# Kernel tuning notes

Hardware: AMD Instinct MI355X
Metric: run time of the kernel (lower is better)

Reference implementation:

```python
import jax, jax.numpy as jnp
import numpy as np

N = 100000      # nodes
E = 1600000     # edges (avg degree 16)
F_IN = 128      # node feature dim
F_E = 8         # edge feature dim
H = 4           # attention heads (layer 1)
C = 16          # hidden per head
T = 1           # target size (layer 2, heads=1, concat=False)
NEG_SLOPE = 0.2


def setup_inputs() -> dict:
    key = jax.random.key(0)
    ks = jax.random.split(key, 20)
    g = lambda k, shape, fan: (jax.random.normal(k, shape, jnp.float32) / np.sqrt(fan))
    return {
        "x": jax.random.normal(ks[0], (N, F_IN), jnp.float32),
        "edge_index": jax.random.randint(ks[1], (2, E), 0, N, dtype=jnp.int32),
        "edge_attr": jax.random.normal(ks[2], (E, F_E), jnp.float32),
        # layer 1 (in=F_IN, out=C, heads=H, concat=True, edge_dim=F_E)
        "Wl1": g(ks[3], (F_IN, H * C), F_IN),
        "bl1": jnp.zeros((H * C,), jnp.float32),
        "Wr1": g(ks[4], (F_IN, H * C), F_IN),
        "br1": jnp.zeros((H * C,), jnp.float32),
        "We1": g(ks[5], (F_E, H * C), F_E),
        "att1": g(ks[6], (H, C), C),
        "b1": jnp.zeros((H * C,), jnp.float32),
        # layer 2 (in=H*C, out=T, heads=1, concat=False, edge_dim=F_E)
        "Wl2": g(ks[7], (H * C, T), H * C),
        "bl2": jnp.zeros((T,), jnp.float32),
        "Wr2": g(ks[8], (H * C, T), H * C),
        "br2": jnp.zeros((T,), jnp.float32),
        "We2": g(ks[9], (F_E, T), F_E),
        "att2": g(ks[10], (1, T), T),
        "b2": jnp.zeros((T,), jnp.float32),
    }


def _gatv2(x, src, dst, eattr, Wl, bl, Wr, br, We, att, bias, heads, out_ch, concat, n_nodes):
    # add self loops, self-loop edge_attr = mean of edge_attr (PyG fill_value='mean')
    loop = jnp.arange(n_nodes, dtype=src.dtype)
    src_a = jnp.concatenate([src, loop])
    dst_a = jnp.concatenate([dst, loop])
    ea = jnp.concatenate(
        [eattr, jnp.broadcast_to(eattr.mean(axis=0), (n_nodes, eattr.shape[1]))], axis=0)

    xl = (x @ Wl + bl).reshape(n_nodes, heads, out_ch)   # source transform
    xr = (x @ Wr + br).reshape(n_nodes, heads, out_ch)   # target transform
    ee = (ea @ We).reshape(-1, heads, out_ch)            # edge transform (no bias)

    # GATv2: score = att . LeakyReLU(x_l[src] + x_r[dst] + W_e e)
    s = jax.nn.leaky_relu(xl[src_a] + xr[dst_a] + ee, NEG_SLOPE)  # [Ea,H,C]
    logits = jnp.einsum('ehc,hc->eh', s, att)                      # [Ea,H]

    # segment softmax over destination nodes (every node has a self loop)
    m = jax.ops.segment_max(logits, dst_a, num_segments=n_nodes)   # [N,H]
    p = jnp.exp(logits - m[dst_a])
    denom = jax.ops.segment_sum(p, dst_a, num_segments=n_nodes)
    alpha = p / denom[dst_a]                                        # [Ea,H]

    out = jax.ops.segment_sum(xl[src_a] * alpha[:, :, None], dst_a,
                              num_segments=n_nodes)                 # [N,H,C]
    out = out.reshape(n_nodes, heads * out_ch) if concat else out.mean(axis=1)
    return out + bias


def reference(x, edge_index, edge_attr, Wl1, bl1, Wr1, br1, We1, att1, b1,
              Wl2, bl2, Wr2, br2, We2, att2, b2):
    src, dst = edge_index[0], edge_index[1]
    # dropout layers are identity at eval time (training=False)
    h = _gatv2(x, src, dst, edge_attr, Wl1, bl1, Wr1, br1, We1, att1, b1,
               H, C, True, N)
    h = jax.nn.elu(h)
    out = _gatv2(h, src, dst, edge_attr, Wl2, bl2, Wr2, br2, We2, att2, b2,
                 1, T, False, N)
    return out
```

## Files before the change

### kernel.cpp

```cpp
#include <hip/hip_runtime.h>
#include <hip/hip_fp16.h>
#include <math.h>

#define N_NODES 100000
#define N_EDGES 1600000
#define N_ITEMS (N_EDGES + N_NODES)
#define F_IN 128
#define HC 64
#define NEG 0.2f
#define SCAN_BS 1024
#define SCAN_NB ((N_NODES + SCAN_BS - 1) / SCAN_BS)
#define MS_BLOCKS 1024

union H2I { __half2 h; int i; };
typedef int v2i __attribute__((ext_vector_type(2)));
typedef int v4i __attribute__((ext_vector_type(4)));

__device__ __forceinline__ float4 h4_to_f4(v2i w) {
    H2I u0, u1; u0.i = w.x; u1.i = w.y;
    float2 a = __half22float2(u0.h), b = __half22float2(u1.h);
    return make_float4(a.x, a.y, b.x, b.y);
}
__device__ __forceinline__ float4 h8_lo(v4i r) {
    H2I h0, h1; h0.i = r.x; h1.i = r.y;
    float2 f0 = __half22float2(h0.h), f1 = __half22float2(h1.h);
    return make_float4(f0.x, f0.y, f1.x, f1.y);
}
__device__ __forceinline__ float4 h8_hi(v4i r) {
    H2I h2, h3; h2.i = r.z; h3.i = r.w;
    float2 f2 = __half22float2(h2.h), f3 = __half22float2(h3.h);
    return make_float4(f2.x, f2.y, f3.x, f3.y);
}

__global__ void mean_sum_kernel(const float* __restrict__ ea, const int* __restrict__ dst,
                                float* __restrict__ partials, unsigned* __restrict__ deg) {
    __shared__ float sh[4][8];
    int stride = gridDim.x * blockDim.x;
    float acc[8] = {0.f,0.f,0.f,0.f,0.f,0.f,0.f,0.f};
    for (int r = blockIdx.x * blockDim.x + threadIdx.x; r < N_EDGES; r += stride) {
        const float4* p = (const float4*)(ea + (size_t)r * 8);
        float4 a = p[0], b = p[1];
        acc[0] += a.x; acc[1] += a.y; acc[2] += a.z; acc[3] += a.w;
        acc[4] += b.x; acc[5] += b.y; acc[6] += b.z; acc[7] += b.w;
        atomicAdd(&deg[dst[r]], 1u);
    }
    int wid  = threadIdx.x >> 6;
    int lane = threadIdx.x & 63;
#pragma unroll
    for (int k = 0; k < 8; k++) {
        float v = acc[k];
        for (int off = 32; off; off >>= 1) v += __shfl_down(v, off);
        if (lane == 0) sh[wid][k] = v;
    }
    __syncthreads();
    if (threadIdx.x < 8) {
        float s = sh[0][threadIdx.x] + sh[1][threadIdx.x] + sh[2][threadIdx.x] + sh[3][threadIdx.x];
        partials[blockIdx.x * 8 + threadIdx.x] = s;
    }
}

__global__ void scan1(const unsigned* __restrict__ deg, unsigned* __restrict__ local_inc,
                      unsigned* __restrict__ bsum,
                      const float* __restrict__ partials, float* __restrict__ sum8) {
    if (blockIdx.x == 0 && threadIdx.x < 64) {
        int lane = threadIdx.x;
        int c = lane & 7, g = lane >> 3;
        float s = 0.f;
        for (int b = g; b < MS_BLOCKS; b += 8) s += partials[b * 8 + c];
        s += __shfl_xor(s, 8);
        s += __shfl_xor(s, 16);
        s += __shfl_xor(s, 32);
        if (lane < 8) sum8[lane] = s;
    }
    __shared__ unsigned wsum[16];
    int i = blockIdx.x * SCAN_BS + threadIdx.x;
    int lane = threadIdx.x & 63;
    int wid  = threadIdx.x >> 6;
    unsigned v = (i < N_NODES) ? (deg[i] + 1u) : 0u;
    unsigned sc = v;
#pragma unroll
    for (int off = 1; off < 64; off <<= 1) {
        unsigned t = __shfl_up(sc, off);
        if (lane >= off) sc += t;
    }
    if (lane == 63) wsum[wid] = sc;
    __syncthreads();
    if (threadIdx.x < 16) {
        unsigned w = wsum[threadIdx.x];
#pragma unroll
        for (int off = 1; off < 16; off <<= 1) {
            unsigned t = __shfl_up(w, off);
            if ((int)threadIdx.x >= off) w += t;
        }
        wsum[threadIdx.x] = w;
    }
    __syncthreads();
    unsigned base = wid ? wsum[wid - 1] : 0u;
    sc += base;
    if (i < N_NODES) local_inc[i] = sc;
    if (threadIdx.x == SCAN_BS - 1) bsum[blockIdx.x] = sc;
}

__global__ void scan23(const unsigned* __restrict__ local_inc, const unsigned* __restrict__ deg,
                       const unsigned* __restrict__ bsum,
                       unsigned* __restrict__ row_start, unsigned* __restrict__ next) {
    __shared__ unsigned tmp[128];
    int t = threadIdx.x;
    if (t < 128) tmp[t] = (t < SCAN_NB) ? bsum[t] : 0u;
    __syncthreads();
    for (int off = 1; off < 128; off <<= 1) {
        unsigned add = 0u;
        if (t < 128 && t >= off) add = tmp[t - off];
        __syncthreads();
        if (t < 128) tmp[t] += add;
        __syncthreads();
    }
    int i = blockIdx.x * blockDim.x + t;
    if (i >= N_NODES) return;
    int b = i >> 10;
    unsigned base = b ? tmp[b - 1] : 0u;
    unsigned v = local_inc[i] - (deg[i] + 1u) + base;
    row_start[i] = v;
    next[i] = v;
}

__global__ void scatter_kernel(const int* __restrict__ src, const int* __restrict__ dst,
                               const float* __restrict__ ea, const float* __restrict__ sum8,
                               const float* __restrict__ We2,
                               unsigned* __restrict__ next,
                               int* __restrict__ rec, __half* __restrict__ seah) {
    int item = blockIdx.x * blockDim.x + threadIdx.x;
    if (item >= N_ITEMS) return;
    int s, d;
    float4 a, b;
    if (item < N_EDGES) {
        s = src[item]; d = dst[item];
        const float4* p = (const float4*)(ea + (size_t)item * 8);
        a = p[0]; b = p[1];
    } else {
        s = d = item - N_EDGES;
        const float inv = 1.0f / N_EDGES;
        a = make_float4(sum8[0]*inv, sum8[1]*inv, sum8[2]*inv, sum8[3]*inv);
        b = make_float4(sum8[4]*inv, sum8[5]*inv, sum8[6]*inv, sum8[7]*inv);
    }
    float ee2 = a.x*We2[0] + a.y*We2[1] + a.z*We2[2] + a.w*We2[3]
              + b.x*We2[4] + b.y*We2[5] + b.z*We2[6] + b.w*We2[7];
    unsigned pos = atomicAdd(&next[d], 1u);
    v2i rr; rr.x = s; rr.y = __float_as_int(ee2);
    *(v2i*)(rec + (size_t)pos * 2) = rr;
    H2I p0, p1, p2, p3;
    p0.h = __floats2half2_rn(a.x, a.y);
    p1.h = __floats2half2_rn(a.z, a.w);
    p2.h = __floats2half2_rn(b.x, b.y);
    p3.h = __floats2half2_rn(b.z, b.w);
    *(int4*)(seah + (size_t)pos * 8) = make_int4(p0.i, p1.i, p2.i, p3.i);
}

__global__ __launch_bounds__(256) void gemm1_kernel(
        const float* __restrict__ x,
        const float* __restrict__ Wl, const float* __restrict__ bl,
        const float* __restrict__ Wr, const float* __restrict__ br,
        __half* __restrict__ xlh, float* __restrict__ xr) {
    __shared__ float xs_t[F_IN][36];
    int t = threadIdx.x & 31;
    int g = threadIdx.x >> 5;
    const float* Wsel = (t < 16) ? Wl : Wr;
    const float* bsel = (t < 16) ? bl : br;
    int jc = (t < 16) ? 4 * t : 4 * t - HC;
    float4 bias = *(const float4*)(bsel + jc);

    int n0 = blockIdx.x * 32;
    int row = threadIdx.x >> 3;
    int cq  = threadIdx.x & 7;
#pragma unroll
    for (int r = 0; r < 4; r++) {
        int c = cq * 4 + r * 32;
        float4 v = *(const float4*)(x + (size_t)(n0 + row) * F_IN + c);
        xs_t[c + 0][row] = v.x;
        xs_t[c + 1][row] = v.y;
        xs_t[c + 2][row] = v.z;
        xs_t[c + 3][row] = v.w;
    }
    __syncthreads();
    int nb = g * 4;
    float4 a0 = bias, a1 = bias, a2 = bias, a3 = bias;
#pragma unroll 4
    for (int k = 0; k < F_IN; k++) {
        float4 w  = *(const float4*)(Wsel + k * HC + jc);
        float4 xv = *(const float4*)&xs_t[k][nb];
        a0.x += w.x * xv.x; a0.y += w.y * xv.x; a0.z += w.z * xv.x; a0.w += w.w * xv.x;
        a1.x += w.x * xv.y; a1.y += w.y * xv.y; a1.z += w.z * xv.y; a1.w += w.w * xv.y;
        a2.x += w.x * xv.z; a2.y += w.y * xv.z; a2.z += w.z * xv.z; a2.w += w.w * xv.z;
        a3.x += w.x * xv.w; a3.y += w.y * xv.w; a3.z += w.z * xv.w; a3.w += w.w * xv.w;
    }
    if (t < 16) {
        float4 arr[4] = {a0, a1, a2, a3};
#pragma unroll
        for (int r = 0; r < 4; r++) {
            H2I u0, u1;
            u0.h = __floats2half2_rn(arr[r].x, arr[r].y);
            u1.h = __floats2half2_rn(arr[r].z, arr[r].w);
            *(int2*)(xlh + (size_t)(n0 + nb + r) * HC + jc) = make_int2(u0.i, u1.i);
        }
    } else {
        *(float4*)(xr + (size_t)(n0 + nb + 0) * HC + jc) = a0;
        *(float4*)(xr + (size_t)(n0 + nb + 1) * HC + jc) = a1;
        *(float4*)(xr + (size_t)(n0 + nb + 2) * HC + jc) = a2;
        *(float4*)(xr + (size_t)(n0 + nb + 3) * HC + jc) = a3;
    }
}

__device__ __forceinline__ void edge_update_nm(const float4* __restrict__ we,
                                               const float4& attv, const float4& xrv,
                                               bool valid, const float4& ea0, const float4& ea1,
                                               const float4& xlv,
                                               float& den, float4& acc) {
    float4 v;
    v.x = xlv.x + xrv.x + ea0.x*we[0].x + ea0.y*we[1].x + ea0.z*we[2].x + ea0.w*we[3].x
                        + ea1.x*we[4].x + ea1.y*we[5].x + ea1.z*we[6].x + ea1.w*we[7].x;
    v.y = xlv.y + xrv.y + ea0.x*we[0].y + ea0.y*we[1].y + ea0.z*we[2].y + ea0.w*we[3].y
                        + ea1.x*we[4].y + ea1.y*we[5].y + ea1.z*we[6].y + ea1.w*we[7].y;
    v.z = xlv.z + xrv.z + ea0.x*we[0].z + ea0.y*we[1].z + ea0.z*we[2].z + ea0.w*we[3].z
                        + ea1.x*we[4].z + ea1.y*we[5].z + ea1.z*we[6].z + ea1.w*we[7].z;
    v.w = xlv.w + xrv.w + ea0.x*we[0].w + ea0.y*we[1].w + ea0.z*we[2].w + ea0.w*we[3].w
                        + ea1.x*we[4].w + ea1.y*we[5].w + ea1.z*we[6].w + ea1.w*we[7].w;
    v.x = fmaxf(v.x, NEG * v.x);
    v.y = fmaxf(v.y, NEG * v.y);
    v.z = fmaxf(v.z, NEG * v.z);
    v.w = fmaxf(v.w, NEG * v.w);
    float prod = v.x*attv.x + v.y*attv.y + v.z*attv.z + v.w*attv.w;
    prod += __shfl_xor(prod, 1);
    prod += __shfl_xor(prod, 2);
    float p = valid ? __expf(prod) : 0.f;
    den   += p;
    acc.x += p * xlv.x;
    acc.y += p * xlv.y;
    acc.z += p * xlv.z;
    acc.w += p * xlv.w;
}

__global__ void gat1_kernel(const unsigned* __restrict__ row_start, const unsigned* __restrict__ deg,
                            const int* __restrict__ rec, const __half* __restrict__ seah,
                            const float* __restrict__ We1, const float* __restrict__ att1,
                            const float* __restrict__ b1,
                            const __half* __restrict__ xlh, const float* __restrict__ xr,
                            const float* __restrict__ Wl2, const float* __restrict__ bl2,
                            const float* __restrict__ Wr2, const float* __restrict__ br2,
                            float* __restrict__ xl2, float* __restrict__ xr2) {
    int node = blockIdx.x * (blockDim.x >> 6) + (threadIdx.x >> 6);
    int lane = threadIdx.x & 63;
    if (node >= N_NODES) return;
    int g  = lane >> 4;
    int cl = lane & 15;
    unsigned start = row_start[node];
    unsigned cnt   = deg[node] + 1u;
    unsigned cm1   = cnt - 1u;

    float4 we[8];
#pragma unroll
    for (int k = 0; k < 8; k++) we[k] = *(const float4*)(We1 + k * HC + 4 * cl);
    float4 attv = *(const float4*)(att1 + 4 * cl);
    float4 xrv  = *(const float4*)(xr + (size_t)node * HC + 4 * cl);

    float denA = 0.f, denB = 0.f;
    float4 accA = make_float4(0.f,0.f,0.f,0.f), accB = make_float4(0.f,0.f,0.f,0.f);

#define IDXA(J) (start + min((J) + (unsigned)g, cm1))
#define IDXB(J) (start + min((J) + 4u + (unsigned)g, cm1))
    unsigned iA = IDXA(0u), iB = IDXB(0u);
    v2i rA = __builtin_nontemporal_load((const v2i*)(rec + (size_t)iA * 2));
    v2i rB = __builtin_nontemporal_load((const v2i*)(rec + (size_t)iB * 2));
    v4i spA = __builtin_nontemporal_load((const v4i*)(seah + (size_t)iA * 8));
    v4i spB = __builtin_nontemporal_load((const v4i*)(seah + (size_t)iB * 8));
    v2i xpA = *(const v2i*)(xlh + (size_t)rA.x * HC + 4 * cl);
    v2i xpB = *(const v2i*)(xlh + (size_t)rB.x * HC + 4 * cl);

    for (unsigned j = 0; j < cnt; j += 8) {
        float4 e0A = h8_lo(spA), e1A = h8_hi(spA), xA = h4_to_f4(xpA);
        float4 e0B = h8_lo(spB), e1B = h8_hi(spB), xB = h4_to_f4(xpB);
        bool vA = (j + g) < cnt, vB = (j + 4 + g) < cnt;
        if (j + 8 < cnt) {
            iA = IDXA(j + 8); iB = IDXB(j + 8);
            rA = __builtin_nontemporal_load((const v2i*)(rec + (size_t)iA * 2));
            rB = __builtin_nontemporal_load((const v2i*)(rec + (size_t)iB * 2));
            spA = __builtin_nontemporal_load((const v4i*)(seah + (size_t)iA * 8));
            spB = __builtin_nontemporal_load((const v4i*)(seah + (size_t)iB * 8));
            xpA = *(const v2i*)(xlh + (size_t)rA.x * HC + 4 * cl);
            xpB = *(const v2i*)(xlh + (size_t)rB.x * HC + 4 * cl);
        }
        edge_update_nm(we, attv, xrv, vA, e0A, e1A, xA, denA, accA);
        edge_update_nm(we, attv, xrv, vB, e0B, e1B, xB, denB, accB);
    }
#undef IDXA
#undef IDXB

    float den = denA + denB;
    float4 acc;
    acc.x = accA.x + accB.x;
    acc.y = accA.y + accB.y;
    acc.z = accA.z + accB.z;
    acc.w = accA.w + accB.w;

    den   += __shfl_xor(den, 16);   den   += __shfl_xor(den, 32);
    acc.x += __shfl_xor(acc.x, 16); acc.x += __shfl_xor(acc.x, 32);
    acc.y += __shfl_xor(acc.y, 16); acc.y += __shfl_xor(acc.y, 32);
    acc.z += __shfl_xor(acc.z, 16); acc.z += __shfl_xor(acc.z, 32);
    acc.w += __shfl_xor(acc.w, 16); acc.w += __shfl_xor(acc.w, 32);

    float4 b1v  = *(const float4*)(b1 + 4 * cl);
    float4 wl2v = *(const float4*)(Wl2 + 4 * cl);
    float4 wr2v = *(const float4*)(Wr2 + 4 * cl);
    float inv_den = 1.f / den;
    float4 o;
    o.x = acc.x * inv_den + b1v.x;
    o.y = acc.y * inv_den + b1v.y;
    o.z = acc.z * inv_den + b1v.z;
    o.w = acc.w * inv_den + b1v.w;
    o.x = o.x > 0.f ? o.x : __expf(o.x) - 1.f;
    o.y = o.y > 0.f ? o.y : __expf(o.y) - 1.f;
    o.z = o.z > 0.f ? o.z : __expf(o.z) - 1.f;
    o.w = o.w > 0.f ? o.w : __expf(o.w) - 1.f;
    float sl = o.x*wl2v.x + o.y*wl2v.y + o.z*wl2v.z + o.w*wl2v.w;
    float sr = o.x*wr2v.x + o.y*wr2v.y + o.z*wr2v.z + o.w*wr2v.w;
#pragma unroll
    for (int off = 1; off <= 8; off <<= 1) {
        sl += __shfl_xor(sl, off);
        sr += __shfl_xor(sr, off);
    }
    if (lane == 0) {
        xl2[node] = sl + bl2[0];
        xr2[node] = sr + br2[0];
    }
}

__global__ __launch_bounds__(256) void gat2_kernel(
        const unsigned* __restrict__ row_start, const unsigned* __restrict__ deg,
        const int* __restrict__ rec, const float* __restrict__ att2,
        const float* __restrict__ xl2, const float* __restrict__ xr2,
        const float* __restrict__ b2, float* __restrict__ out) {
    int wave = threadIdx.x >> 6;
    int lane = threadIdx.x & 63;
    int sub  = lane >> 4;
    int l    = lane & 15;
    int node = (blockIdx.x * 4 + wave) * 4 + sub;
    unsigned start = row_start[node];
    unsigned cnt   = deg[node] + 1u;
    float xrv = xr2[node];
    float a2  = att2[0];
    float den = 0.f, num = 0.f;
    for (unsigned idx = (unsigned)l; idx < cnt; idx += 16) {
        v2i r = __builtin_nontemporal_load((const v2i*)(rec + (size_t)(start + idx) * 2));
        float ee = __int_as_float(r.y);
        float xv = xl2[r.x];
        float v = xv + xrv + ee;
        v = fmaxf(v, NEG * v);
        float p = __expf(a2 * v);
        den += p;
        num += p * xv;
    }
#pragma unroll
    for (int off = 1; off <= 8; off <<= 1) {
        den += __shfl_xor(den, off);
        num += __shfl_xor(num, off);
    }
    if (l == 0) out[node] = num / den + b2[0];
}

extern "C" void kernel_launch(void* const* d_in, const int* in_sizes, int n_in,
                              void* d_out, int out_size, void* d_ws, size_t ws_size,
                              hipStream_t stream) {
    const float* x    = (const float*)d_in[0];
    const int*   ei   = (const int*)d_in[1];
    const float* ea   = (const float*)d_in[2];
    const float* Wl1  = (const float*)d_in[3];
    const float* bl1  = (const float*)d_in[4];
    const float* Wr1  = (const float*)d_in[5];
    const float* br1  = (const float*)d_in[6];
    const float* We1  = (const float*)d_in[7];
    const float* att1 = (const float*)d_in[8];
    const float* b1   = (const float*)d_in[9];
    const float* Wl2  = (const float*)d_in[10];
    const float* bl2  = (const float*)d_in[11];
    const float* Wr2  = (const float*)d_in[12];
    const float* br2  = (const float*)d_in[13];
    const float* We2  = (const float*)d_in[14];
    const float* att2 = (const float*)d_in[15];
    const float* b2   = (const float*)d_in[16];

    const int* src = ei;
    const int* dst = ei + N_EDGES;

    float* W = (float*)d_ws;
    size_t o = 0;
    float*    sum8      = W + o;               o += 8;
    float*    partials  = W + o;               o += MS_BLOCKS * 8;
    unsigned* deg       = (unsigned*)(W + o);  o += N_NODES;
    unsigned* local_inc = (unsigned*)(W + o);  o += N_NODES;
    unsigned* bsum      = (unsigned*)(W + o);  o += 128;
    unsigned* row_start = (unsigned*)(W + o);  o += N_NODES;
    unsigned* next      = (unsigned*)(W + o);  o += N_NODES;
    o = (o + 3) & ~(size_t)3;
    int*      rec       = (int*)(W + o);       o += (size_t)N_ITEMS * 2;
    __half*   seah      = (__half*)(W + o);    o += (size_t)N_ITEMS * 4;
    __half*   xlh       = (__half*)(W + o);    o += (size_t)N_NODES * (HC/2);
    float*    xr1       = W + o;               o += (size_t)N_NODES * HC;
    float*    xl2       = W + o;               o += N_NODES;
    float*    xr2       = W + o;               o += N_NODES;

    hipMemsetAsync(deg, 0, (size_t)N_NODES * sizeof(unsigned), stream);
    mean_sum_kernel<<<MS_BLOCKS, 256, 0, stream>>>(ea, dst, partials, deg);
    scan1<<<SCAN_NB, SCAN_BS, 0, stream>>>(deg, local_inc, bsum, partials, sum8);
    scan23<<<(N_NODES + 255) / 256, 256, 0, stream>>>(local_inc, deg, bsum, row_start, next);
    scatter_kernel<<<(N_ITEMS + 255) / 256, 256, 0, stream>>>(
        src, dst, ea, sum8, We2, next, rec, seah);
    gemm1_kernel<<<N_NODES / 32, 256, 0, stream>>>(x, Wl1, bl1, Wr1, br1, xlh, xr1);
    gat1_kernel<<<(N_NODES + 3) / 4, 256, 0, stream>>>(
        row_start, deg, rec, seah, We1, att1, b1, xlh, xr1,
        Wl2, bl2, Wr2, br2, xl2, xr2);
    gat2_kernel<<<N_NODES / 16, 256, 0, stream>>>(
        row_start, deg, rec, att2, xl2, xr2, b2, (float*)d_out);
}
```

Before: 445.2 us.

## Pack edge records into one 32-byte struct and compute GAT1 edge math in packed fp16

The separate src/ee2 record array and fp16 edge-attribute array are merged into one 32-byte interleaved record per edge, so each edge takes one contiguous fetch. The xr table is stored in fp16 instead of fp32. The GAT1 per-edge projection, LeakyReLU and attention dot product now use packed half2 FMA and v_pk_max_f16 instead of fp32 math. This cuts memory traffic and ALU work, but fp16 accumulation of logits may lose accuracy. gat2 now reads a 32-byte-strided record for an 8-byte payload, which wastes bandwidth.

```diff
diff --git a/kernel.cpp b/kernel.cpp
--- a/kernel.cpp
+++ b/kernel.cpp
@@ -16,20 +16,10 @@
 typedef int v2i __attribute__((ext_vector_type(2)));
 typedef int v4i __attribute__((ext_vector_type(4)));
 
-__device__ __forceinline__ float4 h4_to_f4(v2i w) {
-    H2I u0, u1; u0.i = w.x; u1.i = w.y;
-    float2 a = __half22float2(u0.h), b = __half22float2(u1.h);
-    return make_float4(a.x, a.y, b.x, b.y);
-}
-__device__ __forceinline__ float4 h8_lo(v4i r) {
-    H2I h0, h1; h0.i = r.x; h1.i = r.y;
-    float2 f0 = __half22float2(h0.h), f1 = __half22float2(h1.h);
-    return make_float4(f0.x, f0.y, f1.x, f1.y);
-}
-__device__ __forceinline__ float4 h8_hi(v4i r) {
-    H2I h2, h3; h2.i = r.z; h3.i = r.w;
-    float2 f2 = __half22float2(h2.h), f3 = __half22float2(h3.h);
-    return make_float4(f2.x, f2.y, f3.x, f3.y);
+__device__ __forceinline__ __half2 hmax2(__half2 a, __half2 b) {
+    H2I ua, ub, uc; ua.h = a; ub.h = b;
+    asm("v_pk_max_f16 %0, %1, %2" : "=v"(uc.i) : "v"(ua.i), "v"(ub.i));
+    return uc.h;
 }
 
 __global__ void mean_sum_kernel(const float* __restrict__ ea, const int* __restrict__ dst,
@@ -128,7 +118,7 @@
                                const float* __restrict__ ea, const float* __restrict__ sum8,
                                const float* __restrict__ We2,
                                unsigned* __restrict__ next,
-                               int* __restrict__ rec, __half* __restrict__ seah) {
+                               int* __restrict__ rec32) {
     int item = blockIdx.x * blockDim.x + threadIdx.x;
     if (item >= N_ITEMS) return;
     int s, d;
@@ -146,21 +136,23 @@
     float ee2 = a.x*We2[0] + a.y*We2[1] + a.z*We2[2] + a.w*We2[3]
               + b.x*We2[4] + b.y*We2[5] + b.z*We2[6] + b.w*We2[7];
     unsigned pos = atomicAdd(&next[d], 1u);
-    v2i rr; rr.x = s; rr.y = __float_as_int(ee2);
-    *(v2i*)(rec + (size_t)pos * 2) = rr;
-    H2I p0, p1, p2, p3;
-    p0.h = __floats2half2_rn(a.x, a.y);
-    p1.h = __floats2half2_rn(a.z, a.w);
-    p2.h = __floats2half2_rn(b.x, b.y);
-    p3.h = __floats2half2_rn(b.z, b.w);
-    *(int4*)(seah + (size_t)pos * 8) = make_int4(p0.i, p1.i, p2.i, p3.i);
+    H2I e01, e23, e45, e67;
+    e01.h = __floats2half2_rn(a.x, a.y);
+    e23.h = __floats2half2_rn(a.z, a.w);
+    e45.h = __floats2half2_rn(b.x, b.y);
+    e67.h = __floats2half2_rn(b.z, b.w);
+    int* base = rec32 + (size_t)pos * 8;
+    v4i st1; st1.x = s; st1.y = __float_as_int(ee2); st1.z = e01.i; st1.w = e23.i;
+    *(v4i*)base = st1;
+    v2i st2; st2.x = e45.i; st2.y = e67.i;
+    *(v2i*)(base + 4) = st2;
 }
 
 __global__ __launch_bounds__(256) void gemm1_kernel(
         const float* __restrict__ x,
         const float* __restrict__ Wl, const float* __restrict__ bl,
         const float* __restrict__ Wr, const float* __restrict__ br,
-        __half* __restrict__ xlh, float* __restrict__ xr) {
+        __half* __restrict__ xlh, __half* __restrict__ xrh) {
     __shared__ float xs_t[F_IN][36];
     int t = threadIdx.x & 31;
     int g = threadIdx.x >> 5;
@@ -168,6 +160,7 @@
     const float* bsel = (t < 16) ? bl : br;
     int jc = (t < 16) ? 4 * t : 4 * t - HC;
     float4 bias = *(const float4*)(bsel + jc);
+    __half* table = (t < 16) ? xlh : xrh;
 
     int n0 = blockIdx.x * 32;
     int row = threadIdx.x >> 3;
@@ -193,57 +186,58 @@
         a2.x += w.x * xv.z; a2.y += w.y * xv.z; a2.z += w.z * xv.z; a2.w += w.w * xv.z;
         a3.x += w.x * xv.w; a3.y += w.y * xv.w; a3.z += w.z * xv.w; a3.w += w.w * xv.w;
     }
-    if (t < 16) {
-        float4 arr[4] = {a0, a1, a2, a3};
-#pragma unroll
-        for (int r = 0; r < 4; r++) {
-            H2I u0, u1;
-            u0.h = __floats2half2_rn(arr[r].x, arr[r].y);
-            u1.h = __floats2half2_rn(arr[r].z, arr[r].w);
-            *(int2*)(xlh + (size_t)(n0 + nb + r) * HC + jc) = make_int2(u0.i, u1.i);
-        }
-    } else {
-        *(float4*)(xr + (size_t)(n0 + nb + 0) * HC + jc) = a0;
-        *(float4*)(xr + (size_t)(n0 + nb + 1) * HC + jc) = a1;
-        *(float4*)(xr + (size_t)(n0 + nb + 2) * HC + jc) = a2;
-        *(float4*)(xr + (size_t)(n0 + nb + 3) * HC + jc) = a3;
-    }
-}
-
-__device__ __forceinline__ void edge_update_nm(const float4* __restrict__ we,
-                                               const float4& attv, const float4& xrv,
-                                               bool valid, const float4& ea0, const float4& ea1,
-                                               const float4& xlv,
-                                               float& den, float4& acc) {
-    float4 v;
-    v.x = xlv.x + xrv.x + ea0.x*we[0].x + ea0.y*we[1].x + ea0.z*we[2].x + ea0.w*we[3].x
-                        + ea1.x*we[4].x + ea1.y*we[5].x + ea1.z*we[6].x + ea1.w*we[7].x;
-    v.y = xlv.y + xrv.y + ea0.x*we[0].y + ea0.y*we[1].y + ea0.z*we[2].y + ea0.w*we[3].y
-                        + ea1.x*we[4].y + ea1.y*we[5].y + ea1.z*we[6].y + ea1.w*we[7].y;
-    v.z = xlv.z + xrv.z + ea0.x*we[0].z + ea0.y*we[1].z + ea0.z*we[2].z + ea0.w*we[3].z
-                        + ea1.x*we[4].z + ea1.y*we[5].z + ea1.z*we[6].z + ea1.w*we[7].z;
-    v.w = xlv.w + xrv.w + ea0.x*we[0].w + ea0.y*we[1].w + ea0.z*we[2].w + ea0.w*we[3].w
-                        + ea1.x*we[4].w + ea1.y*we[5].w + ea1.z*we[6].w + ea1.w*we[7].w;
-    v.x = fmaxf(v.x, NEG * v.x);
-    v.y = fmaxf(v.y, NEG * v.y);
-    v.z = fmaxf(v.z, NEG * v.z);
-    v.w = fmaxf(v.w, NEG * v.w);
-    float prod = v.x*attv.x + v.y*attv.y + v.z*attv.z + v.w*attv.w;
+    float4 arr[4] = {a0, a1, a2, a3};
+#pragma unroll
+    for (int r = 0; r < 4; r++) {
+        H2I u0, u1;
+        u0.h = __floats2half2_rn(arr[r].x, arr[r].y);
+        u1.h = __floats2half2_rn(arr[r].z, arr[r].w);
+        *(int2*)(table + (size_t)(n0 + nb + r) * HC + jc) = make_int2(u0.i, u1.i);
+    }
+}
+
+__device__ __forceinline__ void edge_update_h(const __half2* __restrict__ weA,
+                                              const __half2* __restrict__ weB,
+                                              __half2 attA, __half2 attB,
+                                              __half2 xr2a, __half2 xr2b,
+                                              bool valid, v4i L1, v2i L2, v2i xp,
+                                              float& den, float4& acc) {
+    H2I ea01, ea23, ea45, ea67, xl01, xl23;
+    ea01.i = L1.z; ea23.i = L1.w; ea45.i = L2.x; ea67.i = L2.y;
+    xl01.i = xp.x; xl23.i = xp.y;
+    __half2 va = __hadd2(xl01.h, xr2a);
+    __half2 vb = __hadd2(xl23.h, xr2b);
+    __half2 e;
+    e = __low2half2(ea01.h);  va = __hfma2(e, weA[0], va); vb = __hfma2(e, weB[0], vb);
+    e = __high2half2(ea01.h); va = __hfma2(e, weA[1], va); vb = __hfma2(e, weB[1], vb);
+    e = __low2half2(ea23.h);  va = __hfma2(e, weA[2], va); vb = __hfma2(e, weB[2], vb);
+    e = __high2half2(ea23.h); va = __hfma2(e, weA[3], va); vb = __hfma2(e, weB[3], vb);
+    e = __low2half2(ea45.h);  va = __hfma2(e, weA[4], va); vb = __hfma2(e, weB[4], vb);
+    e = __high2half2(ea45.h); va = __hfma2(e, weA[5], va); vb = __hfma2(e, weB[5], vb);
+    e = __low2half2(ea67.h);  va = __hfma2(e, weA[6], va); vb = __hfma2(e, weB[6], vb);
+    e = __high2half2(ea67.h); va = __hfma2(e, weA[7], va); vb = __hfma2(e, weB[7], vb);
+    const __half2 k02 = __float2half2_rn(NEG);
+    va = hmax2(va, __hmul2(va, k02));
+    vb = hmax2(vb, __hmul2(vb, k02));
+    __half2 pd = __hfma2(vb, attB, __hmul2(va, attA));
+    float2 pf = __half22float2(pd);
+    float prod = pf.x + pf.y;
     prod += __shfl_xor(prod, 1);
     prod += __shfl_xor(prod, 2);
     float p = valid ? __expf(prod) : 0.f;
+    float2 xa = __half22float2(xl01.h), xb = __half22float2(xl23.h);
     den   += p;
-    acc.x += p * xlv.x;
-    acc.y += p * xlv.y;
-    acc.z += p * xlv.z;
-    acc.w += p * xlv.w;
+    acc.x += p * xa.x;
+    acc.y += p * xa.y;
+    acc.z += p * xb.x;
+    acc.w += p * xb.y;
 }
 
 __global__ void gat1_kernel(const unsigned* __restrict__ row_start, const unsigned* __restrict__ deg,
-                            const int* __restrict__ rec, const __half* __restrict__ seah,
+                            const int* __restrict__ rec32,
                             const float* __restrict__ We1, const float* __restrict__ att1,
                             const float* __restrict__ b1,
-                            const __half* __restrict__ xlh, const float* __restrict__ xr,
+                            const __half* __restrict__ xlh, const __half* __restrict__ xrh,
                             const float* __restrict__ Wl2, const float* __restrict__ bl2,
                             const float* __restrict__ Wr2, const float* __restrict__ br2,
                             float* __restrict__ xl2, float* __restrict__ xr2) {
@@ -256,11 +250,19 @@
     unsigned cnt   = deg[node] + 1u;
     unsigned cm1   = cnt - 1u;
 
-    float4 we[8];
-#pragma unroll
-    for (int k = 0; k < 8; k++) we[k] = *(const float4*)(We1 + k * HC + 4 * cl);
-    float4 attv = *(const float4*)(att1 + 4 * cl);
-    float4 xrv  = *(const float4*)(xr + (size_t)node * HC + 4 * cl);
+    __half2 weA[8], weB[8];
+#pragma unroll
+    for (int k = 0; k < 8; k++) {
+        float4 w = *(const float4*)(We1 + k * HC + 4 * cl);
+        weA[k] = __floats2half2_rn(w.x, w.y);
+        weB[k] = __floats2half2_rn(w.z, w.w);
+    }
+    float4 at = *(const float4*)(att1 + 4 * cl);
+    __half2 attA = __floats2half2_rn(at.x, at.y);
+    __half2 attB = __floats2half2_rn(at.z, at.w);
+    v2i xrp = *(const v2i*)(xrh + (size_t)node * HC + 4 * cl);
+    H2I xru0, xru1; xru0.i = xrp.x; xru1.i = xrp.y;
+    __half2 xr2a = xru0.h, xr2b = xru1.h;
 
     float denA = 0.f, denB = 0.f;
     float4 accA = make_float4(0.f,0.f,0.f,0.f), accB = make_float4(0.f,0.f,0.f,0.f);
@@ -268,28 +270,28 @@
 #define IDXA(J) (start + min((J) + (unsigned)g, cm1))
 #define IDXB(J) (start + min((J) + 4u + (unsigned)g, cm1))
     unsigned iA = IDXA(0u), iB = IDXB(0u);
-    v2i rA = __builtin_nontemporal_load((const v2i*)(rec + (size_t)iA * 2));
-    v2i rB = __builtin_nontemporal_load((const v2i*)(rec + (size_t)iB * 2));
-    v4i spA = __builtin_nontemporal_load((const v4i*)(seah + (size_t)iA * 8));
-    v4i spB = __builtin_nontemporal_load((const v4i*)(seah + (size_t)iB * 8));
-    v2i xpA = *(const v2i*)(xlh + (size_t)rA.x * HC + 4 * cl);
-    v2i xpB = *(const v2i*)(xlh + (size_t)rB.x * HC + 4 * cl);
+    v4i L1A = __builtin_nontemporal_load((const v4i*)(rec32 + (size_t)iA * 8));
+    v4i L1B = __builtin_nontemporal_load((const v4i*)(rec32 + (size_t)iB * 8));
+    v2i L2A = __builtin_nontemporal_load((const v2i*)(rec32 + (size_t)iA * 8 + 4));
+    v2i L2B = __builtin_nontemporal_load((const v2i*)(rec32 + (size_t)iB * 8 + 4));
+    v2i xpA = *(const v2i*)(xlh + (size_t)L1A.x * HC + 4 * cl);
+    v2i xpB = *(const v2i*)(xlh + (size_t)L1B.x * HC + 4 * cl);
 
     for (unsigned j = 0; j < cnt; j += 8) {
-        float4 e0A = h8_lo(spA), e1A = h8_hi(spA), xA = h4_to_f4(xpA);
-        float4 e0B = h8_lo(spB), e1B = h8_hi(spB), xB = h4_to_f4(xpB);
+        v4i c1A = L1A, c1B = L1B;
+        v2i c2A = L2A, c2B = L2B, cxA = xpA, cxB = xpB;
         bool vA = (j + g) < cnt, vB = (j + 4 + g) < cnt;
         if (j + 8 < cnt) {
             iA = IDXA(j + 8); iB = IDXB(j + 8);
-            rA = __builtin_nontemporal_load((const v2i*)(rec + (size_t)iA * 2));
-            rB = __builtin_nontemporal_load((const v2i*)(rec + (size_t)iB * 2));
-            spA = __builtin_nontemporal_load((const v4i*)(seah + (size_t)iA * 8));
-            spB = __builtin_nontemporal_load((const v4i*)(seah + (size_t)iB * 8));
-            xpA = *(const v2i*)(xlh + (size_t)rA.x * HC + 4 * cl);
-            xpB = *(const v2i*)(xlh + (size_t)rB.x * HC + 4 * cl);
+            L1A = __builtin_nontemporal_load((const v4i*)(rec32 + (size_t)iA * 8));
+            L1B = __builtin_nontemporal_load((const v4i*)(rec32 + (size_t)iB * 8));
+            L2A = __builtin_nontemporal_load((const v2i*)(rec32 + (size_t)iA * 8 + 4));
+            L2B = __builtin_nontemporal_load((const v2i*)(rec32 + (size_t)iB * 8 + 4));
+            xpA = *(const v2i*)(xlh + (size_t)L1A.x * HC + 4 * cl);
+            xpB = *(const v2i*)(xlh + (size_t)L1B.x * HC + 4 * cl);
         }
-        edge_update_nm(we, attv, xrv, vA, e0A, e1A, xA, denA, accA);
-        edge_update_nm(we, attv, xrv, vB, e0B, e1B, xB, denB, accB);
+        edge_update_h(weA, weB, attA, attB, xr2a, xr2b, vA, c1A, c2A, cxA, denA, accA);
+        edge_update_h(weA, weB, attA, attB, xr2a, xr2b, vB, c1B, c2B, cxB, denB, accB);
     }
 #undef IDXA
 #undef IDXB
@@ -335,7 +337,7 @@
 
 __global__ __launch_bounds__(256) void gat2_kernel(
         const unsigned* __restrict__ row_start, const unsigned* __restrict__ deg,
-        const int* __restrict__ rec, const float* __restrict__ att2,
+        const int* __restrict__ rec32, const float* __restrict__ att2,
         const float* __restrict__ xl2, const float* __restrict__ xr2,
         const float* __restrict__ b2, float* __restrict__ out) {
     int wave = threadIdx.x >> 6;
@@ -349,7 +351,7 @@
     float a2  = att2[0];
     float den = 0.f, num = 0.f;
     for (unsigned idx = (unsigned)l; idx < cnt; idx += 16) {
-        v2i r = __builtin_nontemporal_load((const v2i*)(rec + (size_t)(start + idx) * 2));
+        v2i r = __builtin_nontemporal_load((const v2i*)(rec32 + (size_t)(start + idx) * 8));
         float ee = __int_as_float(r.y);
         float xv = xl2[r.x];
         float v = xv + xrv + ee;
@@ -399,11 +401,10 @@
     unsigned* bsum      = (unsigned*)(W + o);  o += 128;
     unsigned* row_start = (unsigned*)(W + o);  o += N_NODES;
     unsigned* next      = (unsigned*)(W + o);  o += N_NODES;
-    o = (o + 3) & ~(size_t)3;
-    int*      rec       = (int*)(W + o);       o += (size_t)N_ITEMS * 2;
-    __half*   seah      = (__half*)(W + o);    o += (size_t)N_ITEMS * 4;
+    o = (o + 7) & ~(size_t)7;
+    int*      rec32     = (int*)(W + o);       o += (size_t)N_ITEMS * 8;
     __half*   xlh       = (__half*)(W + o);    o += (size_t)N_NODES * (HC/2);
-    float*    xr1       = W + o;               o += (size_t)N_NODES * HC;
+    __half*   xrh       = (__half*)(W + o);    o += (size_t)N_NODES * (HC/2);
     float*    xl2       = W + o;               o += N_NODES;
     float*    xr2       = W + o;               o += N_NODES;
 
@@ -412,11 +413,11 @@
     scan1<<<SCAN_NB, SCAN_BS, 0, stream>>>(deg, local_inc, bsum, partials, sum8);
     scan23<<<(N_NODES + 255) / 256, 256, 0, stream>>>(local_inc, deg, bsum, row_start, next);
     scatter_kernel<<<(N_ITEMS + 255) / 256, 256, 0, stream>>>(
-        src, dst, ea, sum8, We2, next, rec, seah);
-    gemm1_kernel<<<N_NODES / 32, 256, 0, stream>>>(x, Wl1, bl1, Wr1, br1, xlh, xr1);
+        src, dst, ea, sum8, We2, next, rec32);
+    gemm1_kernel<<<N_NODES / 32, 256, 0, stream>>>(x, Wl1, bl1, Wr1, br1, xlh, xrh);
     gat1_kernel<<<(N_NODES + 3) / 4, 256, 0, stream>>>(
-        row_start, deg, rec, seah, We1, att1, b1, xlh, xr1,
+        row_start, deg, rec32, We1, att1, b1, xlh, xrh,
         Wl2, bl2, Wr2, br2, xl2, xr2);
     gat2_kernel<<<N_NODES / 16, 256, 0, stream>>>(
-        row_start, deg, rec, att2, xl2, xr2, b2, (float*)d_out);
-}
+        row_start, deg, rec32, att2, xl2, xr2, b2, (float*)d_out);
+}
```

After: 405.8 us. -8.9%, faster.
